# Kernel tuning notes

Hardware: AMD Instinct MI355X
Metric: run time of the kernel (lower is better)

Reference implementation:

```python
import jax, jax.numpy as jnp
import numpy as np

B, S, H = 64, 2048, 1024
X0, X1, X2, A = 1024, 512, 512, 512


def setup_inputs() -> dict:
    key = jax.random.key(0)
    ks = jax.random.split(key, 11)
    wb = np.sqrt(6.0 / (H + A)).astype(np.float32)
    w0b = np.sqrt(6.0 / (X0 + A)).astype(np.float32)
    w1b = np.sqrt(6.0 / (X1 + A)).astype(np.float32)
    w2b = np.sqrt(6.0 / (X2 + A)).astype(np.float32)
    return {
        "hidden_states": jax.random.normal(ks[0], (B, S, H), dtype=jnp.float32),
        "x0_hidden_states": jax.random.normal(ks[1], (B, X0), dtype=jnp.float32),
        "x1_hidden_states": jax.random.normal(ks[2], (B, X1), dtype=jnp.float32),
        "x2_hidden_states": jax.random.normal(ks[3], (B, X2), dtype=jnp.float32),
        "lengths": jax.random.randint(ks[4], (B,), 1, S + 1),
        # torch Linear stores weight as [out, in]
        "Wh_w": jax.random.uniform(ks[5], (A, H), minval=-wb, maxval=wb, dtype=jnp.float32),
        "Wh_b": jnp.zeros((A,), dtype=jnp.float32),
        "W0_w": jax.random.uniform(ks[6], (A, X0), minval=-w0b, maxval=w0b, dtype=jnp.float32),
        "W1_w": jax.random.uniform(ks[7], (A, X1), minval=-w1b, maxval=w1b, dtype=jnp.float32),
        "W2_w": jax.random.uniform(ks[8], (A, X2), minval=-w2b, maxval=w2b, dtype=jnp.float32),
        "V_w": 0.1 * jax.random.normal(ks[9], (1, A), dtype=jnp.float32),
    }


def reference(hidden_states, x0_hidden_states, x1_hidden_states, x2_hidden_states,
              lengths, Wh_w, Wh_b, W0_w, W1_w, W2_w, V_w):
    # Ah: [B,S,A]; context projections broadcast over seq dim
    Ah = jnp.einsum('bsh,ah->bsa', hidden_states, Wh_w) + Wh_b
    A0 = (x0_hidden_states @ W0_w.T)[:, None, :]
    A1 = (x1_hidden_states @ W1_w.T)[:, None, :]
    A2 = (x2_hidden_states @ W2_w.T)[:, None, :]
    w = jax.nn.relu(Ah + A0 + A1 + A2)
    scores = jnp.einsum('bsa,a->bs', w, V_w[0])  # [B,S]
    mask = jnp.arange(scores.shape[1])[None, :] < lengths[:, None]
    scores = jnp.where(mask, scores, -jnp.inf)
    attention_prob = jax.nn.softmax(scores, axis=1)
    output = jnp.einsum('bs,bsh->bh', attention_prob, hidden_states)
    return output, attention_prob
```

## Files before the change

kernel.cpp:

```cpp
#include <hip/hip_runtime.h>
#include <stdint.h>

#define B_ 64
#define S_ 2048
#define H_ 1024
#define X0_ 1024
#define X1_ 512
#define X2_ 512
#define A_ 512

typedef __attribute__((ext_vector_type(8))) short short8;
typedef __attribute__((ext_vector_type(8))) __bf16 bf16x8;
typedef __attribute__((ext_vector_type(4))) float floatx4;

typedef __attribute__((address_space(1))) const void glb_cv;
typedef __attribute__((address_space(3))) void lds_v;

__device__ inline unsigned short f2bf(float f) {
    union { float f; unsigned u; } v; v.f = f;
    unsigned u = v.u;
    unsigned r = u + 0x7FFF + ((u >> 16) & 1);
    return (unsigned short)(r >> 16);
}

__global__ void k_convert_wh(const float* __restrict__ wh, unsigned short* __restrict__ whb) {
    int i = (blockIdx.x * 256 + threadIdx.x) * 4;
    float4 f = *(const float4*)(wh + i);
    ushort4 o;
    o.x = f2bf(f.x); o.y = f2bf(f.y); o.z = f2bf(f.z); o.w = f2bf(f.w);
    *(ushort4*)(whb + i) = o;
}

__global__ void k_convert_h(const float* __restrict__ hidden, const int* __restrict__ lengths,
                            unsigned short* __restrict__ hbf) {
    int b = blockIdx.x >> 8;
    int r0 = (blockIdx.x & 255) * 8;
    if (r0 >= lengths[b]) return;
    int t = threadIdx.x;
    const float* src = hidden + ((size_t)(b * S_ + r0)) * H_ + t * 4;
    unsigned short* dst = hbf + ((size_t)(b * S_ + r0)) * H_ + t * 4;
#pragma unroll
    for (int i = 0; i < 8; i++) {
        float4 f = *(const float4*)(src + (size_t)i * H_);
        ushort4 o;
        o.x = f2bf(f.x); o.y = f2bf(f.y); o.z = f2bf(f.z); o.w = f2bf(f.w);
        *(ushort4*)(dst + (size_t)i * H_) = o;
    }
}

__global__ void k_ctx(const float* __restrict__ x0, const float* __restrict__ x1,
                      const float* __restrict__ x2, const float* __restrict__ w0,
                      const float* __restrict__ w1, const float* __restrict__ w2,
                      const float* __restrict__ bias, float* __restrict__ ctx) {
    __shared__ float xs[X0_ + X1_ + X2_];
    int b = blockIdx.x >> 4;
    int a0 = (blockIdx.x & 15) << 5;
    int t = threadIdx.x;
    for (int i = t; i < X0_; i += 256) xs[i] = x0[b * X0_ + i];
    for (int i = t; i < X1_; i += 256) xs[X0_ + i] = x1[b * X1_ + i];
    for (int i = t; i < X2_; i += 256) xs[X0_ + X1_ + i] = x2[b * X2_ + i];
    __syncthreads();
    int wave = t >> 6, lane = t & 63;
    for (int j = 0; j < 8; j++) {
        int a = a0 + wave * 8 + j;
        float acc = 0.f;
        const float* r0 = w0 + (size_t)a * X0_;
        for (int k = lane; k < X0_; k += 64) acc += r0[k] * xs[k];
        const float* r1 = w1 + (size_t)a * X1_;
        for (int k = lane; k < X1_; k += 64) acc += r1[k] * xs[X0_ + k];
        const float* r2 = w2 + (size_t)a * X2_;
        for (int k = lane; k < X2_; k += 64) acc += r2[k] * xs[X0_ + X1_ + k];
        for (int off = 32; off; off >>= 1) acc += __shfl_down(acc, off, 64);
        if (lane == 0) ctx[b * A_ + a] = acc + bias[a];
    }
}

__launch_bounds__(256, 2)
__global__ void k_scores(const unsigned short* __restrict__ hbf, const unsigned short* __restrict__ whb,
                         const float* __restrict__ ctx, const float* __restrict__ vw,
                         const int* __restrict__ lengths, float* __restrict__ partial) {
    int b = blockIdx.x >> 6;
    int mt = (blockIdx.x >> 2) & 15;
    int nblk = blockIdx.x & 3;
    int s0 = mt * 128;
    if (s0 >= lengths[b]) return;
    int n0b = nblk * 128;

    __shared__ unsigned short As[128 * 32];
    __shared__ unsigned short Bs[128 * 32];
    __shared__ float sred[4][64];

    int t = threadIdx.x;
    int wv = t >> 6, lane = t & 63;
    int nl = lane & 15, quad = lane >> 4;
    int wm0 = (wv & 1) * 64;
    int wn0 = (wv >> 1) * 64;

    floatx4 acc[4][4];
#pragma unroll
    for (int i = 0; i < 4; i++)
#pragma unroll
        for (int j = 0; j < 4; j++) acc[i][j] = (floatx4){0.f, 0.f, 0.f, 0.f};

    const unsigned short* abase = hbf + (size_t)(b * S_ + s0) * H_;
    const unsigned short* bbase = whb + (size_t)n0b * H_;

    for (int k0 = 0; k0 < H_; k0 += 32) {
#pragma unroll
        for (int i = 0; i < 2; i++) {
            int c = wv * 64 + i * 256 + lane;
            const unsigned short* ga = abase + (size_t)(c >> 2) * H_ + k0 + (c & 3) * 8;
            __builtin_amdgcn_global_load_lds((glb_cv*)ga,
                (lds_v*)(As + (wv * 64 + i * 256) * 8), 16, 0, 0);
        }
#pragma unroll
        for (int i = 0; i < 2; i++) {
            int c = wv * 64 + i * 256 + lane;
            const unsigned short* gb = bbase + (size_t)(c >> 2) * H_ + k0 + (c & 3) * 8;
            __builtin_amdgcn_global_load_lds((glb_cv*)gb,
                (lds_v*)(Bs + (wv * 64 + i * 256) * 8), 16, 0, 0);
        }
        __syncthreads();

        short8 af[4];
#pragma unroll
        for (int m = 0; m < 4; m++)
            af[m] = *(const short8*)&As[(wm0 + m * 16 + nl) * 32 + quad * 8];
#pragma unroll
        for (int n = 0; n < 4; n++) {
            short8 bfr = *(const short8*)&Bs[(wn0 + n * 16 + nl) * 32 + quad * 8];
            bf16x8 bfv = __builtin_bit_cast(bf16x8, bfr);
#pragma unroll
            for (int m = 0; m < 4; m++) {
                bf16x8 afv = __builtin_bit_cast(bf16x8, af[m]);
                acc[m][n] = __builtin_amdgcn_mfma_f32_16x16x32_bf16(afv, bfv, acc[m][n], 0, 0, 0);
            }
        }
        __syncthreads();
    }

    float cv[4], cc[4];
#pragma unroll
    for (int n = 0; n < 4; n++) {
        int gn = n0b + wn0 + n * 16 + nl;
        cv[n] = vw[gn];
        cc[n] = ctx[b * A_ + gn];
    }
#pragma unroll
    for (int m = 0; m < 4; m++) {
#pragma unroll
        for (int r = 0; r < 4; r++) {
            float sv = 0.f;
#pragma unroll
            for (int n = 0; n < 4; n++) {
                float x = acc[m][n][r] + cc[n];
                sv += (x > 0.f) ? x * cv[n] : 0.f;
            }
#pragma unroll
            for (int off = 1; off < 16; off <<= 1) sv += __shfl_xor(sv, off, 16);
            if (nl == 0) sred[wv][m * 16 + quad * 4 + r] = sv;
        }
    }
    __syncthreads();
    if (t < 128) {
        int h = t >> 6;
        float s = sred[h][t & 63] + sred[h + 2][t & 63];
        partial[((size_t)nblk * B_ + b) * S_ + s0 + t] = s;
    }
}

__global__ void k_softmax(const float* __restrict__ partial, const int* __restrict__ lengths,
                          float* __restrict__ scores, float* __restrict__ probs) {
    int b = blockIdx.x;
    int len = lengths[b];
    int t = threadIdx.x;
    __shared__ float red[256];
    float mx = -1e30f;
    for (int s = t; s < len; s += 256) {
        float sc = partial[(size_t)b * S_ + s] + partial[((size_t)B_ + b) * S_ + s] +
                   partial[((size_t)2 * B_ + b) * S_ + s] + partial[((size_t)3 * B_ + b) * S_ + s];
        scores[b * S_ + s] = sc;
        mx = fmaxf(mx, sc);
    }
    red[t] = mx; __syncthreads();
    for (int off = 128; off; off >>= 1) {
        if (t < off) red[t] = fmaxf(red[t], red[t + off]);
        __syncthreads();
    }
    mx = red[0]; __syncthreads();
    float sum = 0.f;
    for (int s = t; s < len; s += 256) sum += __expf(scores[b * S_ + s] - mx);
    red[t] = sum; __syncthreads();
    for (int off = 128; off; off >>= 1) {
        if (t < off) red[t] += red[t + off];
        __syncthreads();
    }
    float inv = 1.f / red[0];
    for (int s = t; s < S_; s += 256)
        probs[b * S_ + s] = (s < len) ? __expf(scores[b * S_ + s] - mx) * inv : 0.f;
}

__global__ void k_weighted(const float* __restrict__ hidden, const float* __restrict__ probs,
                           const int* __restrict__ lengths, float* __restrict__ partial) {
    int blk = blockIdx.x;
    int b = blk >> 4, ch = blk & 15;
    int len = lengths[b];
    int s0 = ch * 128;
    if (s0 >= len) return;
    int send = min(s0 + 128, len);
    int t = threadIdx.x;
    float4 acc = {0.f, 0.f, 0.f, 0.f};
    const float* hb = hidden + (size_t)(b * S_ + s0) * H_ + t * 4;
    const float* pb = probs + b * S_;
    int s = s0;
    for (; s + 1 < send; s += 2) {
        float p0 = pb[s], p1 = pb[s + 1];
        float4 h0 = *(const float4*)hb;
        float4 h1 = *(const float4*)(hb + H_);
        acc.x += p0 * h0.x + p1 * h1.x;
        acc.y += p0 * h0.y + p1 * h1.y;
        acc.z += p0 * h0.z + p1 * h1.z;
        acc.w += p0 * h0.w + p1 * h1.w;
        hb += 2 * H_;
    }
    if (s < send) {
        float p = pb[s];
        float4 h = *(const float4*)hb;
        acc.x += p * h.x; acc.y += p * h.y; acc.z += p * h.z; acc.w += p * h.w;
    }
    *(float4*)(partial + ((size_t)ch * B_ + b) * H_ + t * 4) = acc;
}

__global__ void k_reduce(const float* __restrict__ partial, const int* __restrict__ lengths,
                         float* __restrict__ out) {
    int i = blockIdx.x * 256 + threadIdx.x;
    int b = i >> 10;
    int h = i & 1023;
    int len = lengths[b];
    int nch = (len + 127) >> 7;
    float s = 0.f;
    for (int c = 0; c < nch; c++) s += partial[((size_t)c * B_ + b) * H_ + h];
    out[i] = s;
}

extern "C" void kernel_launch(void* const* d_in, const int* in_sizes, int n_in,
                              void* d_out, int out_size, void* d_ws, size_t ws_size,
                              hipStream_t stream) {
    const float* hidden = (const float*)d_in[0];
    const float* x0 = (const float*)d_in[1];
    const float* x1 = (const float*)d_in[2];
    const float* x2 = (const float*)d_in[3];
    const int* lengths = (const int*)d_in[4];
    const float* wh_w = (const float*)d_in[5];
    const float* wh_b = (const float*)d_in[6];
    const float* w0_w = (const float*)d_in[7];
    const float* w1_w = (const float*)d_in[8];
    const float* w2_w = (const float*)d_in[9];
    const float* v_w = (const float*)d_in[10];

    float* out = (float*)d_out;
    float* probs = out + B_ * H_;

    char* ws = (char*)d_ws;
    float* ctx = (float*)ws;
    unsigned short* whb = (unsigned short*)(ws + (1 << 17));
    float* scores = (float*)(ws + (1 << 17) + (1 << 20));
    float* pscore = (float*)(ws + (1 << 17) + (1 << 20) + (1 << 19));
    float* pout = (float*)(ws + (1 << 17) + (1 << 20) + (1 << 19) + (1 << 21));
    unsigned short* hbf = (unsigned short*)(ws + (1 << 17) + (1 << 20) + (1 << 19) + (1 << 21) + (1 << 22));

    k_convert_wh<<<dim3(A_ * H_ / 1024), dim3(256), 0, stream>>>(wh_w, whb);
    k_convert_h<<<dim3(B_ * 256), dim3(256), 0, stream>>>(hidden, lengths, hbf);
    k_ctx<<<dim3(B_ * (A_ / 32)), dim3(256), 0, stream>>>(x0, x1, x2, w0_w, w1_w, w2_w, wh_b, ctx);
    k_scores<<<dim3(B_ * 64), dim3(256), 0, stream>>>(hbf, whb, ctx, v_w, lengths, pscore);
    k_softmax<<<dim3(B_), dim3(256), 0, stream>>>(pscore, lengths, scores, probs);
    k_weighted<<<dim3(B_ * 16), dim3(256), 0, stream>>>(hidden, probs, lengths, pout);
    k_reduce<<<dim3(B_ * H_ / 256), dim3(256), 0, stream>>>(pout, lengths, out);
}
```

Baseline: 917.4 us.

## Fuse hidden-state bf16 conversion into the scores GEMM A-tile load

Drops the separate pass that converted hidden states to bf16 in a workspace buffer. The scores kernel now loads fp32 hidden rows straight into registers, converts them to bf16 in-kernel and stores them to LDS, prefetching the next K-slice while the MFMAs run. This removes a full read and write of the valid hidden rows plus one launch. In exchange, each of the four N-blocks that share an A-tile reads fp32 instead of bf16, doubling A-side load bytes and adding register pressure.

```diff
diff --git a/kernel.cpp b/kernel.cpp
--- a/kernel.cpp
+++ b/kernel.cpp
@@ -1,4 +1,5 @@
 #include <hip/hip_runtime.h>
+#include <hip/hip_bf16.h>
 #include <stdint.h>
 
 #define B_ 64
@@ -23,29 +24,16 @@
     return (unsigned short)(r >> 16);
 }
 
+__device__ inline short hwbf(float f) {
+    return (short)__builtin_bit_cast(unsigned short, __float2bfloat16(f));
+}
+
 __global__ void k_convert_wh(const float* __restrict__ wh, unsigned short* __restrict__ whb) {
     int i = (blockIdx.x * 256 + threadIdx.x) * 4;
     float4 f = *(const float4*)(wh + i);
     ushort4 o;
     o.x = f2bf(f.x); o.y = f2bf(f.y); o.z = f2bf(f.z); o.w = f2bf(f.w);
     *(ushort4*)(whb + i) = o;
-}
-
-__global__ void k_convert_h(const float* __restrict__ hidden, const int* __restrict__ lengths,
-                            unsigned short* __restrict__ hbf) {
-    int b = blockIdx.x >> 8;
-    int r0 = (blockIdx.x & 255) * 8;
-    if (r0 >= lengths[b]) return;
-    int t = threadIdx.x;
-    const float* src = hidden + ((size_t)(b * S_ + r0)) * H_ + t * 4;
-    unsigned short* dst = hbf + ((size_t)(b * S_ + r0)) * H_ + t * 4;
-#pragma unroll
-    for (int i = 0; i < 8; i++) {
-        float4 f = *(const float4*)(src + (size_t)i * H_);
-        ushort4 o;
-        o.x = f2bf(f.x); o.y = f2bf(f.y); o.z = f2bf(f.z); o.w = f2bf(f.w);
-        *(ushort4*)(dst + (size_t)i * H_) = o;
-    }
 }
 
 __global__ void k_ctx(const float* __restrict__ x0, const float* __restrict__ x1,
@@ -76,7 +64,7 @@
 }
 
 __launch_bounds__(256, 2)
-__global__ void k_scores(const unsigned short* __restrict__ hbf, const unsigned short* __restrict__ whb,
+__global__ void k_scores(const float* __restrict__ hidden, const unsigned short* __restrict__ whb,
                          const float* __restrict__ ctx, const float* __restrict__ vw,
                          const int* __restrict__ lengths, float* __restrict__ partial) {
     int b = blockIdx.x >> 6;
@@ -96,23 +84,25 @@
     int wm0 = (wv & 1) * 64;
     int wn0 = (wv >> 1) * 64;
 
+    int c0 = wv * 64 + lane;
+    int c1 = c0 + 256;
+    const float* abase = hidden + (size_t)(b * S_ + s0) * H_;
+    const unsigned short* bbase = whb + (size_t)n0b * H_;
+    size_t aoff0 = (size_t)(c0 >> 2) * H_ + (c0 & 3) * 8;
+    size_t aoff1 = (size_t)(c1 >> 2) * H_ + (c1 & 3) * 8;
+
+    float4 a0a = *(const float4*)(abase + aoff0);
+    float4 a0b = *(const float4*)(abase + aoff0 + 4);
+    float4 a1a = *(const float4*)(abase + aoff1);
+    float4 a1b = *(const float4*)(abase + aoff1 + 4);
+
     floatx4 acc[4][4];
 #pragma unroll
     for (int i = 0; i < 4; i++)
 #pragma unroll
         for (int j = 0; j < 4; j++) acc[i][j] = (floatx4){0.f, 0.f, 0.f, 0.f};
 
-    const unsigned short* abase = hbf + (size_t)(b * S_ + s0) * H_;
-    const unsigned short* bbase = whb + (size_t)n0b * H_;
-
     for (int k0 = 0; k0 < H_; k0 += 32) {
-#pragma unroll
-        for (int i = 0; i < 2; i++) {
-            int c = wv * 64 + i * 256 + lane;
-            const unsigned short* ga = abase + (size_t)(c >> 2) * H_ + k0 + (c & 3) * 8;
-            __builtin_amdgcn_global_load_lds((glb_cv*)ga,
-                (lds_v*)(As + (wv * 64 + i * 256) * 8), 16, 0, 0);
-        }
 #pragma unroll
         for (int i = 0; i < 2; i++) {
             int c = wv * 64 + i * 256 + lane;
@@ -120,7 +110,21 @@
             __builtin_amdgcn_global_load_lds((glb_cv*)gb,
                 (lds_v*)(Bs + (wv * 64 + i * 256) * 8), 16, 0, 0);
         }
-        __syncthreads();
+        short8 pa, pb;
+        pa[0] = hwbf(a0a.x); pa[1] = hwbf(a0a.y); pa[2] = hwbf(a0a.z); pa[3] = hwbf(a0a.w);
+        pa[4] = hwbf(a0b.x); pa[5] = hwbf(a0b.y); pa[6] = hwbf(a0b.z); pa[7] = hwbf(a0b.w);
+        pb[0] = hwbf(a1a.x); pb[1] = hwbf(a1a.y); pb[2] = hwbf(a1a.z); pb[3] = hwbf(a1a.w);
+        pb[4] = hwbf(a1b.x); pb[5] = hwbf(a1b.y); pb[6] = hwbf(a1b.z); pb[7] = hwbf(a1b.w);
+        *(short8*)&As[c0 * 8] = pa;
+        *(short8*)&As[c1 * 8] = pb;
+        __syncthreads();
+
+        if (k0 + 32 < H_) {
+            a0a = *(const float4*)(abase + aoff0 + k0 + 32);
+            a0b = *(const float4*)(abase + aoff0 + k0 + 36);
+            a1a = *(const float4*)(abase + aoff1 + k0 + 32);
+            a1b = *(const float4*)(abase + aoff1 + k0 + 36);
+        }
 
         short8 af[4];
 #pragma unroll
@@ -267,12 +271,10 @@
     float* scores = (float*)(ws + (1 << 17) + (1 << 20));
     float* pscore = (float*)(ws + (1 << 17) + (1 << 20) + (1 << 19));
     float* pout = (float*)(ws + (1 << 17) + (1 << 20) + (1 << 19) + (1 << 21));
-    unsigned short* hbf = (unsigned short*)(ws + (1 << 17) + (1 << 20) + (1 << 19) + (1 << 21) + (1 << 22));
 
     k_convert_wh<<<dim3(A_ * H_ / 1024), dim3(256), 0, stream>>>(wh_w, whb);
-    k_convert_h<<<dim3(B_ * 256), dim3(256), 0, stream>>>(hidden, lengths, hbf);
     k_ctx<<<dim3(B_ * (A_ / 32)), dim3(256), 0, stream>>>(x0, x1, x2, w0_w, w1_w, w2_w, wh_b, ctx);
-    k_scores<<<dim3(B_ * 64), dim3(256), 0, stream>>>(hbf, whb, ctx, v_w, lengths, pscore);
+    k_scores<<<dim3(B_ * 64), dim3(256), 0, stream>>>(hidden, whb, ctx, v_w, lengths, pscore);
     k_softmax<<<dim3(B_), dim3(256), 0, stream>>>(pscore, lengths, scores, probs);
     k_weighted<<<dim3(B_ * 16), dim3(256), 0, stream>>>(hidden, probs, lengths, pout);
     k_reduce<<<dim3(B_ * H_ / 256), dim3(256), 0, stream>>>(pout, lengths, out);
```

New measurement: 886.4 us. -3.4%, faster.
